# Kernel tuning notes

Measured on AMD Instinct MI355X. Metric: run time of the kernel, lower is better.

## Reference

```python
import jax, jax.numpy as jnp
import numpy as np

N, D_IN, D_OUT = 4096, 1024, 1024

def setup_inputs() -> dict:
    key = jax.random.key(0)
    ks = jax.random.split(key, 7)
    s = 1.0 / np.sqrt(D_IN)
    return {
        "x": jax.random.normal(ks[0], (N, D_IN), dtype=jnp.float32),
        "W1": jax.random.normal(ks[1], (D_OUT, D_IN), dtype=jnp.float32) * s,
        "b1": jax.random.normal(ks[2], (D_OUT,), dtype=jnp.float32) * 0.01,
        "W2": jax.random.normal(ks[3], (D_OUT, D_IN), dtype=jnp.float32) * s,
        "b2": jax.random.normal(ks[4], (D_OUT,), dtype=jnp.float32) * 0.01,
        "W3": jax.random.normal(ks[5], (D_OUT, D_IN), dtype=jnp.float32) * s,
        "b3": jax.random.normal(ks[6], (D_OUT,), dtype=jnp.float32) * 0.01,
        "output_dim": D_OUT,
    }

def reference(x, W1, b1, W2, b2, W3, b3, output_dim):
    # q, k, v: [N, D_OUT]  (torch Linear: x @ W.T + b)
    q = x @ W1.T + b1
    k = x @ W2.T + b2
    v = x @ W3.T + b3
    # NOTE: original computes K @ Q^T (not Q @ K^T) — keep faithful.
    scale = 1.0 / jnp.sqrt(jnp.asarray(output_dim, dtype=x.dtype))
    attn = jax.nn.softmax(jnp.einsum("nd,md->nm", k, q) * scale, axis=-1)  # [N, N]
    # value.unsqueeze(0) * attn.unsqueeze(-1) summed over axis 1 == attn @ v
    return attn @ v  # [N, D_OUT]
```

## Files before the change

### kernel.cpp

```cpp
#include <hip/hip_runtime.h>


typedef short bf16x8 __attribute__((ext_vector_type(8)));
typedef float f32x4  __attribute__((ext_vector_type(4)));

__device__ __forceinline__ short f2bf(float f) {
    unsigned u = __builtin_bit_cast(unsigned, f);
    u += 0x7FFFu + ((u >> 16) & 1u);
    return (short)(u >> 16);
}
__device__ __forceinline__ float bf2f(short s) {
    return __builtin_bit_cast(float, (unsigned)((unsigned short)s) << 16);
}

__device__ __forceinline__ void gld_lds16(const short* g, short* l) {
    __builtin_amdgcn_global_load_lds(
        (const __attribute__((address_space(1))) void*)g,
        (__attribute__((address_space(3))) void*)l, 16, 0, 0);
}

template<int BM, int BN>
__global__ __launch_bounds__(256)
void gemm_bt(const short* __restrict__ A, int lda,
             const short* __restrict__ B, int ldb,
             const float* __restrict__ bias,
             short* __restrict__ Cout, int ldc, int cmode, float scale,
             int K, size_t zstride)
{
    constexpr int NT = BN / 32;
    __shared__ __align__(16) short As[BM * 64];
    __shared__ __align__(16) short Bs[BN * 64];

    const int tid  = threadIdx.x;
    const int lane = tid & 63;
    const int wave = tid >> 6;
    const int wm   = (wave >> 1) * 64;
    const int wn   = (wave & 1) * (BN / 2);
    const int quad = lane >> 4;
    const int l16  = lane & 15;
    const size_t bm0 = (size_t)blockIdx.y * BM;
    const size_t bn0 = (size_t)blockIdx.x * BN;
    const int koff = blockIdx.z * K;

    f32x4 acc[4][NT] = {};

    const int srow = lane >> 3;
    const int scol = ((lane & 7) ^ srow) << 3;
    const short* Ag = A + (bm0 + srow) * (size_t)lda + koff + scol;
    const short* Bg = B + (bn0 + srow) * (size_t)ldb + koff + scol;

    for (int k0 = 0; k0 < K; k0 += 64) {
#pragma unroll
        for (int cc = 0; cc < BM / 8; cc += 4) {
            const int c = cc + wave;
            gld_lds16(Ag + (size_t)c * 8 * lda + k0, &As[c * 512]);
        }
#pragma unroll
        for (int cc = 0; cc < BN / 8; cc += 4) {
            const int c = cc + wave;
            gld_lds16(Bg + (size_t)c * 8 * ldb + k0, &Bs[c * 512]);
        }
        __syncthreads();

#pragma unroll
        for (int ks = 0; ks < 2; ks++) {
            const int sw = (ks << 2) + quad;
            bf16x8 af[4], bfr[NT];
#pragma unroll
            for (int mt = 0; mt < 4; mt++) {
                const int r = wm + mt * 16 + l16;
                af[mt] = *(const bf16x8*)(&As[r * 64 + ((sw ^ (r & 7)) << 3)]);
            }
#pragma unroll
            for (int nt = 0; nt < NT; nt++) {
                const int r = wn + nt * 16 + l16;
                bfr[nt] = *(const bf16x8*)(&Bs[r * 64 + ((sw ^ (r & 7)) << 3)]);
            }
#pragma unroll
            for (int mt = 0; mt < 4; mt++)
#pragma unroll
                for (int nt = 0; nt < NT; nt++)
                    acc[mt][nt] = __builtin_amdgcn_mfma_f32_16x16x32_bf16(
                        af[mt], bfr[nt], acc[mt][nt], 0, 0, 0);
        }
        __syncthreads();
    }

    short* Cs = Cout + ((cmode == 3) ? blockIdx.z * zstride : 0);
#pragma unroll
    for (int mt = 0; mt < 4; mt++) {
#pragma unroll
        for (int nt = 0; nt < NT; nt++) {
            const size_t col = bn0 + wn + nt * 16 + l16;
            const float bc = bias ? bias[col] : 0.0f;
#pragma unroll
            for (int r = 0; r < 4; r++) {
                const size_t row = bm0 + wm + mt * 16 + quad * 4 + r;
                float v = acc[mt][nt][r] * scale + bc;
                if (cmode == 2) v = __expf(v);
                Cs[row * (size_t)ldc + col] = f2bf(v);
            }
        }
    }
}

__global__ __launch_bounds__(256)
void transpose_v(const short* __restrict__ qkv, short* __restrict__ vt)
{
    __shared__ short sh[64][72];
    const int n0 = blockIdx.x * 64, d0 = blockIdx.y * 64;
    const int t = threadIdx.x;
    const int r = t >> 2, c = (t & 3) << 4;

    const short* src = qkv + (size_t)(n0 + r) * 3072 + 2048 + d0 + c;
    *(int4*)(&sh[r][c])     = *(const int4*)(src);
    *(int4*)(&sh[r][c + 8]) = *(const int4*)(src + 8);
    __syncthreads();

    short tmp[16];
#pragma unroll
    for (int j = 0; j < 16; j++) tmp[j] = sh[c + j][r];
    short* dst = vt + (size_t)(d0 + r) * 4096 + n0 + c;
    *(int4*)(dst)     = *(const int4*)(tmp);
    *(int4*)(dst + 8) = *(const int4*)(tmp + 8);
}

__global__ __launch_bounds__(256)
void reduce4div(const short* __restrict__ E, const short* __restrict__ outp,
                float* __restrict__ out)
{
    const int row = blockIdx.x;
    const int t = threadIdx.x;
    const int wave = t >> 6, lane = t & 63;

    const short* e = E + (size_t)row * 4096 + (t << 4);
    short sh[16];
    *(int4*)(sh)     = *(const int4*)(e);
    *(int4*)(sh + 8) = *(const int4*)(e + 8);
    float s = 0.0f;
#pragma unroll
    for (int i = 0; i < 16; i++) s += bf2f(sh[i]);
#pragma unroll
    for (int off = 32; off; off >>= 1) s += __shfl_down(s, off);
    __shared__ float red[4];
    if (lane == 0) red[wave] = s;
    __syncthreads();
    const float inv = 1.0f / (red[0] + red[1] + red[2] + red[3]);

    const size_t base = (size_t)row * 1024 + (t << 2);
    float a[4] = {0.0f, 0.0f, 0.0f, 0.0f};
#pragma unroll
    for (int z = 0; z < 4; z++) {
        short4 p = *(const short4*)(outp + z * (size_t)4096 * 1024 + base);
        a[0] += bf2f(p.x); a[1] += bf2f(p.y);
        a[2] += bf2f(p.z); a[3] += bf2f(p.w);
    }
    float4 o;
    o.x = a[0] * inv; o.y = a[1] * inv; o.z = a[2] * inv; o.w = a[3] * inv;
    *(float4*)(out + base) = o;
}

__global__ __launch_bounds__(256)
void prep(const float* __restrict__ x, const float* __restrict__ W1,
          const float* __restrict__ W2, const float* __restrict__ W3,
          const float* __restrict__ b1, const float* __restrict__ b2,
          const float* __restrict__ b3,
          short* __restrict__ xb, short* __restrict__ Wb,
          float* __restrict__ bcat)
{
    const int i = blockIdx.x * 256 + threadIdx.x;
    const int NX = 1048576;
    const int NW = 262144;
    if (i < NX + 3 * NW) {
        const float* src; short* dst; int j;
        if (i < NX)               { src = x;  dst = xb; j = i; }
        else if (i < NX + NW)     { src = W1; dst = Wb; j = i - NX; }
        else if (i < NX + 2 * NW) { src = W2; dst = Wb + 1048576; j = i - NX - NW; }
        else                      { src = W3; dst = Wb + 2097152; j = i - NX - 2 * NW; }
        const float4 f = ((const float4*)src)[j];
        short4 o;
        o.x = f2bf(f.x); o.y = f2bf(f.y); o.z = f2bf(f.z); o.w = f2bf(f.w);
        *(short4*)(dst + (j << 2)) = o;
    } else {
        const int j = i - (NX + 3 * NW);
        if (j < 3072)
            bcat[j] = (j < 1024) ? b1[j] : (j < 2048 ? b2[j - 1024] : b3[j - 2048]);
    }
}

extern "C" void kernel_launch(void* const* d_in, const int* in_sizes, int n_in,
                              void* d_out, int out_size, void* d_ws, size_t ws_size,
                              hipStream_t stream)
{
    const float* x  = (const float*)d_in[0];
    const float* W1 = (const float*)d_in[1];
    const float* b1 = (const float*)d_in[2];
    const float* W2 = (const float*)d_in[3];
    const float* b2 = (const float*)d_in[4];
    const float* W3 = (const float*)d_in[5];
    const float* b3 = (const float*)d_in[6];
    float* out = (float*)d_out;

    const int N = 4096, D = 1024;

    char* wsb = (char*)d_ws;
    short* vt   = (short*)wsb;
    short* E    = (short*)(wsb + (size_t)8  * 1024 * 1024);
    short* xb   = (short*)(wsb + (size_t)40 * 1024 * 1024);
    short* Wb   = (short*)(wsb + (size_t)48 * 1024 * 1024);
    float* bcat = (float*)(wsb + (size_t)54 * 1024 * 1024);
    short* qkv  = (short*)(wsb + (size_t)54 * 1024 * 1024 + 16384);
    short* outp = (short*)(wsb + (size_t)40 * 1024 * 1024);

    prep<<<(1048576 + 3 * 262144 + 3072 + 255) / 256, 256, 0, stream>>>(
        x, W1, W2, W3, b1, b2, b3, xb, Wb, bcat);

    dim3 gqkv(3 * D / 96, N / 128);
    gemm_bt<128, 96><<<gqkv, 256, 0, stream>>>(xb, D, Wb, D, bcat,
                                               qkv, 3 * D, 0, 1.0f, D, 0);

    dim3 gt(N / 64, D / 64);
    transpose_v<<<gt, 256, 0, stream>>>(qkv, vt);

    dim3 gs(N / 128, N / 128);
    gemm_bt<128, 128><<<gs, 256, 0, stream>>>(qkv + D, 3 * D, qkv, 3 * D,
                                              nullptr, E, N, 2, 0.03125f, D, 0);

    dim3 go(D / 128, N / 128, 4);
    gemm_bt<128, 128><<<go, 256, 0, stream>>>(E, N, vt, N, nullptr,
                                              outp, D, 3, 1.0f, N / 4,
                                              (size_t)N * D);

    reduce4div<<<N, 256, 0, stream>>>(E, outp, out);
}
```

Before: 245.4 us.

## Split QKV into separate buffers, swizzle score grid, fp32 two-way split-K output

The QKV projection now writes Q, K and V to separate contiguous buffers, so the score GEMM and the V transpose read with unit stride instead of a 3072-wide interleaved stride. The score GEMM gets an XCD-aware block-index swizzle meant to improve L2 reuse across chiplets. The attention-times-V GEMM changes from a 4-way split-K with bf16 partials to a 2-way split with 128x64 tiles and fp32 partials, and the final reduce kernel sums two fp32 partials. This halves reduction traffic and keeps more precision in the partials, but it launches fewer blocks per split and writes wider data.

```diff
diff --git a/kernel.cpp b/kernel.cpp
--- a/kernel.cpp
+++ b/kernel.cpp
@@ -24,8 +24,8 @@
 void gemm_bt(const short* __restrict__ A, int lda,
              const short* __restrict__ B, int ldb,
              const float* __restrict__ bias,
-             short* __restrict__ Cout, int ldc, int cmode, float scale,
-             int K, size_t zstride)
+             void* __restrict__ Cout, int ldc, int cmode, float scale,
+             int K, size_t zstride, int swz)
 {
     constexpr int NT = BN / 32;
     __shared__ __align__(16) short As[BM * 64];
@@ -38,8 +38,16 @@
     const int wn   = (wave & 1) * (BN / 2);
     const int quad = lane >> 4;
     const int l16  = lane & 15;
-    const size_t bm0 = (size_t)blockIdx.y * BM;
-    const size_t bn0 = (size_t)blockIdx.x * BN;
+
+    int bxx = blockIdx.x, byy = blockIdx.y;
+    if (swz) {
+        const int flat = byy * 32 + bxx;
+        const int xcd = flat & 7, s = flat >> 3;
+        byy = ((xcd >> 2) << 4) + (s & 15);
+        bxx = ((xcd & 3) << 3) + (s >> 4);
+    }
+    const size_t bm0 = (size_t)byy * BM;
+    const size_t bn0 = (size_t)bxx * BN;
     const int koff = blockIdx.z * K;
 
     f32x4 acc[4][NT] = {};
@@ -86,7 +94,8 @@
         __syncthreads();
     }
 
-    short* Cs = Cout + ((cmode == 3) ? blockIdx.z * zstride : 0);
+    float* Cf = (float*)Cout + blockIdx.z * zstride;
+    short* Cs = (short*)Cout;
 #pragma unroll
     for (int mt = 0; mt < 4; mt++) {
 #pragma unroll
@@ -96,23 +105,29 @@
 #pragma unroll
             for (int r = 0; r < 4; r++) {
                 const size_t row = bm0 + wm + mt * 16 + quad * 4 + r;
-                float v = acc[mt][nt][r] * scale + bc;
-                if (cmode == 2) v = __expf(v);
-                Cs[row * (size_t)ldc + col] = f2bf(v);
+                const float v = acc[mt][nt][r] * scale + bc;
+                if (cmode == 1) {
+                    Cf[row * (size_t)ldc + col] = v;
+                } else if (cmode == 2) {
+                    Cs[row * (size_t)ldc + col] = f2bf(__expf(v));
+                } else {
+                    Cs[(col >> 10) * (size_t)4194304 + row * 1024 + (col & 1023)]
+                        = f2bf(v);
+                }
             }
         }
     }
 }
 
 __global__ __launch_bounds__(256)
-void transpose_v(const short* __restrict__ qkv, short* __restrict__ vt)
+void transpose_v(const short* __restrict__ v, short* __restrict__ vt)
 {
     __shared__ short sh[64][72];
     const int n0 = blockIdx.x * 64, d0 = blockIdx.y * 64;
     const int t = threadIdx.x;
     const int r = t >> 2, c = (t & 3) << 4;
 
-    const short* src = qkv + (size_t)(n0 + r) * 3072 + 2048 + d0 + c;
+    const short* src = v + (size_t)(n0 + r) * 1024 + d0 + c;
     *(int4*)(&sh[r][c])     = *(const int4*)(src);
     *(int4*)(&sh[r][c + 8]) = *(const int4*)(src + 8);
     __syncthreads();
@@ -126,7 +141,7 @@
 }
 
 __global__ __launch_bounds__(256)
-void reduce4div(const short* __restrict__ E, const short* __restrict__ outp,
+void reduce2div(const short* __restrict__ E, const float* __restrict__ outp,
                 float* __restrict__ out)
 {
     const int row = blockIdx.x;
@@ -148,15 +163,11 @@
     const float inv = 1.0f / (red[0] + red[1] + red[2] + red[3]);
 
     const size_t base = (size_t)row * 1024 + (t << 2);
-    float a[4] = {0.0f, 0.0f, 0.0f, 0.0f};
-#pragma unroll
-    for (int z = 0; z < 4; z++) {
-        short4 p = *(const short4*)(outp + z * (size_t)4096 * 1024 + base);
-        a[0] += bf2f(p.x); a[1] += bf2f(p.y);
-        a[2] += bf2f(p.z); a[3] += bf2f(p.w);
-    }
+    const float4 a = *(const float4*)(outp + base);
+    const float4 b = *(const float4*)(outp + (size_t)4096 * 1024 + base);
     float4 o;
-    o.x = a[0] * inv; o.y = a[1] * inv; o.z = a[2] * inv; o.w = a[3] * inv;
+    o.x = (a.x + b.x) * inv; o.y = (a.y + b.y) * inv;
+    o.z = (a.z + b.z) * inv; o.w = (a.w + b.w) * inv;
     *(float4*)(out + base) = o;
 }
 
@@ -206,30 +217,32 @@
     char* wsb = (char*)d_ws;
     short* vt   = (short*)wsb;
     short* E    = (short*)(wsb + (size_t)8  * 1024 * 1024);
-    short* xb   = (short*)(wsb + (size_t)40 * 1024 * 1024);
-    short* Wb   = (short*)(wsb + (size_t)48 * 1024 * 1024);
-    float* bcat = (float*)(wsb + (size_t)54 * 1024 * 1024);
-    short* qkv  = (short*)(wsb + (size_t)54 * 1024 * 1024 + 16384);
-    short* outp = (short*)(wsb + (size_t)40 * 1024 * 1024);
+    short* q    = (short*)(wsb + (size_t)40 * 1024 * 1024);
+    short* k    = (short*)(wsb + (size_t)48 * 1024 * 1024);
+    short* v    = (short*)(wsb + (size_t)56 * 1024 * 1024);
+    short* xb   = (short*)(wsb + (size_t)64 * 1024 * 1024);
+    short* Wb   = (short*)(wsb + (size_t)72 * 1024 * 1024);
+    float* bcat = (float*)(wsb + (size_t)78 * 1024 * 1024);
+    float* outp = (float*)(wsb + (size_t)40 * 1024 * 1024);
 
     prep<<<(1048576 + 3 * 262144 + 3072 + 255) / 256, 256, 0, stream>>>(
         x, W1, W2, W3, b1, b2, b3, xb, Wb, bcat);
 
     dim3 gqkv(3 * D / 96, N / 128);
     gemm_bt<128, 96><<<gqkv, 256, 0, stream>>>(xb, D, Wb, D, bcat,
-                                               qkv, 3 * D, 0, 1.0f, D, 0);
+                                               q, 0, 4, 1.0f, D, 0, 0);
 
     dim3 gt(N / 64, D / 64);
-    transpose_v<<<gt, 256, 0, stream>>>(qkv, vt);
+    transpose_v<<<gt, 256, 0, stream>>>(v, vt);
 
     dim3 gs(N / 128, N / 128);
-    gemm_bt<128, 128><<<gs, 256, 0, stream>>>(qkv + D, 3 * D, qkv, 3 * D,
-                                              nullptr, E, N, 2, 0.03125f, D, 0);
-
-    dim3 go(D / 128, N / 128, 4);
-    gemm_bt<128, 128><<<go, 256, 0, stream>>>(E, N, vt, N, nullptr,
-                                              outp, D, 3, 1.0f, N / 4,
-                                              (size_t)N * D);
-
-    reduce4div<<<N, 256, 0, stream>>>(E, outp, out);
-}
+    gemm_bt<128, 128><<<gs, 256, 0, stream>>>(k, D, q, D, nullptr,
+                                              E, N, 2, 0.03125f, D, 0, 1);
+
+    dim3 go(D / 64, N / 128, 2);
+    gemm_bt<128, 64><<<go, 256, 0, stream>>>(E, N, vt, N, nullptr,
+                                             outp, D, 1, 1.0f, N / 2,
+                                             (size_t)N * D, 0);
+
+    reduce2div<<<N, 256, 0, stream>>>(E, outp, out);
+}
```

Result: slower. 260.4 us (+6.1%).
